# Kernel tuning notes

Measured on AMD Instinct MI355X. Metric: run time of the kernel, lower is better.

Reference implementation:

```python
import jax, jax.numpy as jnp
import numpy as np

B, C, D, H, W = 2, 256, 16, 64, 64


def _conv1x1(x, w, b):
    # 1x1x1 Conv3d == pointwise channel matmul. x: [B,C,D,H,W], w: [Cout,Cin], b: [Cout]
    return jnp.einsum('bcdhw,oc->bodhw', x, w) + b[None, :, None, None, None]


def setup_inputs() -> dict:
    key = jax.random.key(0)
    ks = jax.random.split(key, 12)
    wscale = 1.0 / np.sqrt(C)  # keep pre-softmax logits in a sane range
    inp = {
        'eeg_input': jax.random.normal(ks[0], (B, C, D, H, W), jnp.float32),
        'image_input': jax.random.normal(ks[1], (B, C, D, H, W), jnp.float32),
        'q_w': jax.random.normal(ks[2], (C, C), jnp.float32) * wscale,
        'q_b': jnp.zeros((C,), jnp.float32),
        'k_w': jax.random.normal(ks[3], (C, C), jnp.float32) * wscale,
        'k_b': jnp.zeros((C,), jnp.float32),
        'v_w': jax.random.normal(ks[4], (C, C), jnp.float32) * wscale,
        'v_b': jnp.zeros((C,), jnp.float32),
        'attn_w': jax.random.normal(ks[5], (C, C), jnp.float32) * wscale,
        'attn_b': jnp.zeros((C,), jnp.float32),
        'out_w': jax.random.normal(ks[6], (C, C), jnp.float32) * wscale,
        'out_b': jnp.zeros((C,), jnp.float32),
    }
    return inp


def reference(eeg_input, image_input, q_w, q_b, k_w, k_b, v_w, v_b,
              attn_w, attn_b, out_w, out_b):
    q = _conv1x1(eeg_input, q_w, q_b)      # [B,C,D,H,W]
    k = _conv1x1(image_input, k_w, k_b)    # [B,C,D,H,W]
    v = _conv1x1(image_input, v_w, v_b)    # [B,C,D,H,W]
    # torch.matmul(q, k.transpose(-2,-1)): contract over W -> scores [B,C,D,H,H]
    scores = jax.nn.softmax(jnp.einsum('bcdhw,bcdxw->bcdhx', q, k), axis=-1)
    wv = jnp.einsum('bcdhx,bcdxw->bcdhw', scores, v)  # [B,C,D,H,W]
    a = jax.nn.relu(_conv1x1(wv, attn_w, attn_b))
    return jax.nn.relu(_conv1x1(a, out_w, out_b))
```

## Files before the change

### kernel.cpp

```cpp
#include <hip/hip_runtime.h>

#define CC   256
#define DHWC 65536
#define NBC  2

typedef __attribute__((ext_vector_type(8))) short bf16x8;
typedef __attribute__((ext_vector_type(4))) short bf16x4;
typedef __attribute__((ext_vector_type(4))) float f32x4;

__device__ __forceinline__ short f2bf(float x) {
    unsigned u = __builtin_bit_cast(unsigned, x);
    unsigned r = (u + 0x7fffu + ((u >> 16) & 1u)) >> 16;
    return (short)r;
}
__device__ __forceinline__ float bf2f(short h) {
    unsigned u = ((unsigned)(unsigned short)h) << 16;
    return __builtin_bit_cast(float, u);
}

__device__ __forceinline__ int swz(int r, int c) {
    return (r * 128 + c * 2) ^ ((r & 7) << 4);
}
__device__ __forceinline__ int vswz(int r, int c) {
    return (r * 128 + c * 2) ^ (((r ^ (r >> 3)) & 7) << 4);
}
__device__ __forceinline__ int swz512(int s, int k) {
    return (s * 512 + k * 2) ^ ((s & 7) << 4);
}

__global__ void prep_w_kernel(const float* __restrict__ q_w, const float* __restrict__ k_w,
                              const float* __restrict__ v_w, const float* __restrict__ attn_w,
                              const float* __restrict__ out_w, short* __restrict__ wsp)
{
    const int l  = threadIdx.x;
    const int fo = blockIdx.x;
    const int t  = blockIdx.y;
    const int m  = blockIdx.z;
    const float* w = (m == 0) ? q_w : (m == 1) ? k_w : (m == 2) ? v_w
                   : (m == 3) ? attn_w : out_w;
    short* whi = wsp + (size_t)m * 131072;
    short* wlo = whi + 65536;

    const int o = fo * 16 + (l & 15);
    const int k = t * 32 + (l >> 4) * 8;

    bf16x8 hv, lv;
    #pragma unroll
    for (int r = 0; r < 8; ++r) {
        const float x = w[o * 256 + k + r];
        const short h = f2bf(x);
        hv[r] = h;
        lv[r] = f2bf(x - bf2f(h));
    }
    const int idx = (fo * 8 + t) * 64 + l;
    *(bf16x8*)(whi + idx * 8) = hv;
    *(bf16x8*)(wlo + idx * 8) = lv;
}

__global__ __launch_bounds__(1024, 4) void conv_mfma_kernel(
    const float* __restrict__ x, const short* __restrict__ whi,
    const short* __restrict__ wlo, const float* __restrict__ bias,
    float* __restrict__ out, const int do_relu)
{
    __shared__ char lds[65536];

    const int tid  = threadIdx.x;
    const int lane = tid & 63;
    const int wave = tid >> 6;
    const size_t boff = (size_t)blockIdx.y * ((size_t)CC * DHWC);
    const int sT = blockIdx.x * 128;
    const float* xb = x + boff + sT;
    const bf16x8* whf = (const bf16x8*)whi;
    const bf16x8* wlf = (const bf16x8*)wlo;

    f32x4 acc[8];
    #pragma unroll
    for (int j = 0; j < 8; ++j) acc[j] = (f32x4){0.f, 0.f, 0.f, 0.f};

    const int s_l = tid & 127;
    const int k8  = tid >> 7;

    float xr[8];
    #pragma unroll
    for (int r = 0; r < 8; ++r)
        xr[r] = xb[(size_t)(k8 * 8 + r) * DHWC + s_l];
    {
        bf16x8 hv, lv;
        #pragma unroll
        for (int r = 0; r < 8; ++r) {
            const short h = f2bf(xr[r]);
            hv[r] = h;
            lv[r] = f2bf(xr[r] - bf2f(h));
        }
        const int off = swz(s_l, k8 * 8);
        *(bf16x8*)(lds + off) = hv;
        *(bf16x8*)(lds + 16384 + off) = lv;
    }

    #pragma unroll
    for (int t = 0; t < 4; ++t) {
        if (t < 3) {
            #pragma unroll
            for (int r = 0; r < 8; ++r)
                xr[r] = xb[(size_t)((t + 1) * 64 + k8 * 8 + r) * DHWC + s_l];
        }
        __syncthreads();

        const char* bhib = lds + (t & 1) * 32768;
        const char* blob = bhib + 16384;
        #pragma unroll
        for (int kk = 0; kk < 2; ++kk) {
            const int idx = (wave * 8 + 2 * t + kk) * 64 + lane;
            const bf16x8 a1h = whf[idx];
            const bf16x8 a1l = wlf[idx];
            #pragma unroll
            for (int j = 0; j < 8; ++j) {
                const int s = j * 16 + (lane & 15);
                const int k = kk * 32 + (lane >> 4) * 8;
                const bf16x8 bh = *(const bf16x8*)(bhib + swz(s, k));
                const bf16x8 bl = *(const bf16x8*)(blob + swz(s, k));
                f32x4 c = acc[j];
                c = __builtin_amdgcn_mfma_f32_16x16x32_bf16(a1h, bh, c, 0, 0, 0);
                c = __builtin_amdgcn_mfma_f32_16x16x32_bf16(a1h, bl, c, 0, 0, 0);
                c = __builtin_amdgcn_mfma_f32_16x16x32_bf16(a1l, bh, c, 0, 0, 0);
                acc[j] = c;
            }
        }

        if (t < 3) {
            bf16x8 hv, lv;
            #pragma unroll
            for (int r = 0; r < 8; ++r) {
                const short h = f2bf(xr[r]);
                hv[r] = h;
                lv[r] = f2bf(xr[r] - bf2f(h));
            }
            const int off = ((t + 1) & 1) * 32768 + swz(s_l, k8 * 8);
            *(bf16x8*)(lds + off) = hv;
            *(bf16x8*)(lds + 16384 + off) = lv;
        }
    }

    float* ob = out + boff + sT;
    const int n_l = lane & 15;
    const int m4  = (lane >> 4) * 4;
    #pragma unroll
    for (int r = 0; r < 4; ++r) {
        const int o = wave * 16 + m4 + r;
        const float bv = bias[o];
        #pragma unroll
        for (int j = 0; j < 8; ++j) {
            float val = acc[j][r] + bv;
            if (do_relu) val = fmaxf(val, 0.f);
            ob[(size_t)o * DHWC + j * 16 + n_l] = val;
        }
    }
}

__global__ __launch_bounds__(1024, 4) void kv_conv_kernel(
    const float* __restrict__ img,
    const short* __restrict__ wkhi, const short* __restrict__ wklo,
    const short* __restrict__ wvhi, const short* __restrict__ wvlo,
    const float* __restrict__ kb, const float* __restrict__ vb,
    float* __restrict__ kout, short* __restrict__ vout)
{
    __shared__ char lds[65536];

    const int tid  = threadIdx.x;
    const int lane = tid & 63;
    const int wave = tid >> 6;
    const size_t boff = (size_t)blockIdx.y * ((size_t)CC * DHWC);
    const int sT = blockIdx.x * 128;
    const float* xb = img + boff + sT;
    const bf16x8* wkhf = (const bf16x8*)wkhi;
    const bf16x8* wklf = (const bf16x8*)wklo;
    const bf16x8* wvhf = (const bf16x8*)wvhi;
    const bf16x8* wvlf = (const bf16x8*)wvlo;

    f32x4 acck[8], accv[8];
    #pragma unroll
    for (int j = 0; j < 8; ++j) {
        acck[j] = (f32x4){0.f, 0.f, 0.f, 0.f};
        accv[j] = (f32x4){0.f, 0.f, 0.f, 0.f};
    }

    const int s_l = tid & 127;
    const int k8  = tid >> 7;

    float xr[8];
    #pragma unroll
    for (int r = 0; r < 8; ++r)
        xr[r] = xb[(size_t)(k8 * 8 + r) * DHWC + s_l];
    {
        bf16x8 hv, lv;
        #pragma unroll
        for (int r = 0; r < 8; ++r) {
            const short h = f2bf(xr[r]);
            hv[r] = h;
            lv[r] = f2bf(xr[r] - bf2f(h));
        }
        const int off = swz(s_l, k8 * 8);
        *(bf16x8*)(lds + off) = hv;
        *(bf16x8*)(lds + 16384 + off) = lv;
    }

    #pragma unroll
    for (int t = 0; t < 4; ++t) {
        if (t < 3) {
            #pragma unroll
            for (int r = 0; r < 8; ++r)
                xr[r] = xb[(size_t)((t + 1) * 64 + k8 * 8 + r) * DHWC + s_l];
        }
        __syncthreads();

        const char* bhib = lds + (t & 1) * 32768;
        const char* blob = bhib + 16384;
        #pragma unroll
        for (int kk = 0; kk < 2; ++kk) {
            const int idx = (wave * 8 + 2 * t + kk) * 64 + lane;
            const bf16x8 akh = wkhf[idx];
            const bf16x8 akl = wklf[idx];
            const bf16x8 avh = wvhf[idx];
            const bf16x8 avl = wvlf[idx];
            #pragma unroll
            for (int j = 0; j < 8; ++j) {
                const int s = j * 16 + (lane & 15);
                const int k = kk * 32 + (lane >> 4) * 8;
                const bf16x8 bh = *(const bf16x8*)(bhib + swz(s, k));
                const bf16x8 bl = *(const bf16x8*)(blob + swz(s, k));
                f32x4 c = acck[j];
                c = __builtin_amdgcn_mfma_f32_16x16x32_bf16(akh, bh, c, 0, 0, 0);
                c = __builtin_amdgcn_mfma_f32_16x16x32_bf16(akh, bl, c, 0, 0, 0);
                c = __builtin_amdgcn_mfma_f32_16x16x32_bf16(akl, bh, c, 0, 0, 0);
                acck[j] = c;
                f32x4 d = accv[j];
                d = __builtin_amdgcn_mfma_f32_16x16x32_bf16(avh, bh, d, 0, 0, 0);
                d = __builtin_amdgcn_mfma_f32_16x16x32_bf16(avh, bl, d, 0, 0, 0);
                d = __builtin_amdgcn_mfma_f32_16x16x32_bf16(avl, bh, d, 0, 0, 0);
                accv[j] = d;
            }
        }

        if (t < 3) {
            bf16x8 hv, lv;
            #pragma unroll
            for (int r = 0; r < 8; ++r) {
                const short h = f2bf(xr[r]);
                hv[r] = h;
                lv[r] = f2bf(xr[r] - bf2f(h));
            }
            const int off = ((t + 1) & 1) * 32768 + swz(s_l, k8 * 8);
            *(bf16x8*)(lds + off) = hv;
            *(bf16x8*)(lds + 16384 + off) = lv;
        }
    }

    float* ko = kout + boff + sT;
    short* vo = vout + boff + sT;
    const int n_l = lane & 15;
    const int m4  = (lane >> 4) * 4;
    #pragma unroll
    for (int r = 0; r < 4; ++r) {
        const int o = wave * 16 + m4 + r;
        const float kbv = kb[o];
        const float vbv = vb[o];
        #pragma unroll
        for (int j = 0; j < 8; ++j) {
            ko[(size_t)o * DHWC + j * 16 + n_l] = acck[j][r] + kbv;
            vo[(size_t)o * DHWC + j * 16 + n_l] = f2bf(accv[j][r] + vbv);
        }
    }
}

__global__ __launch_bounds__(256, 4) void attn_mfma_kernel(
    const float* q, const float* __restrict__ kg,
    const short* __restrict__ vsh, float* wv)
{
    __shared__ char lds[40960];
    const int QHI = 0, QLO = 8192, KHI = 16384, KLO = 24576, VT = 32768;

    const int tid  = threadIdx.x;
    const int lane = tid & 63;
    const int wsx  = tid >> 6;
    const size_t base = (size_t)blockIdx.x * 4096;

    {
        const int r  = tid >> 2;
        const int cb = (tid & 3) * 16;
        #pragma unroll
        for (int half = 0; half < 2; ++half) {
            const int c = cb + half * 8;
            const float4 qa = *(const float4*)(q  + base + r * 64 + c);
            const float4 qb = *(const float4*)(q  + base + r * 64 + c + 4);
            const float4 ka = *(const float4*)(kg + base + r * 64 + c);
            const float4 kb = *(const float4*)(kg + base + r * 64 + c + 4);
            bf16x8 qh, ql, kh, kl;
            #pragma unroll
            for (int e = 0; e < 4; ++e) {
                float xq = ((const float*)&qa)[e];
                short h = f2bf(xq); qh[e] = h; ql[e] = f2bf(xq - bf2f(h));
                xq = ((const float*)&qb)[e];
                h = f2bf(xq); qh[e + 4] = h; ql[e + 4] = f2bf(xq - bf2f(h));
                float xk = ((const float*)&ka)[e];
                h = f2bf(xk); kh[e] = h; kl[e] = f2bf(xk - bf2f(h));
                xk = ((const float*)&kb)[e];
                h = f2bf(xk); kh[e + 4] = h; kl[e + 4] = f2bf(xk - bf2f(h));
            }
            const int off = swz(r, c);
            *(bf16x8*)(lds + QHI + off) = qh;
            *(bf16x8*)(lds + QLO + off) = ql;
            *(bf16x8*)(lds + KHI + off) = kh;
            *(bf16x8*)(lds + KLO + off) = kl;
        }
        const short* vpl = vsh + base;
        const int x0 = (tid >> 4) * 4;
        const int w0 = (tid & 15) * 4;
        bf16x4 vr[4];
        #pragma unroll
        for (int i = 0; i < 4; ++i)
            vr[i] = *(const bf16x4*)(vpl + (x0 + i) * 64 + w0);
        #pragma unroll
        for (int j = 0; j < 4; ++j) {
            bf16x4 tv;
            #pragma unroll
            for (int i = 0; i < 4; ++i) tv[i] = vr[i][j];
            *(bf16x4*)(lds + VT + vswz(w0 + j, x0)) = tv;
        }
    }
    __syncthreads();

    f32x4 acc[4];
    #pragma unroll
    for (int j = 0; j < 4; ++j) acc[j] = (f32x4){0.f, 0.f, 0.f, 0.f};

    const int arow = wsx * 16 + (lane & 15);
    #pragma unroll
    for (int kk = 0; kk < 2; ++kk) {
        const int kcol = kk * 32 + (lane >> 4) * 8;
        const bf16x8 aqh = *(const bf16x8*)(lds + QHI + swz(arow, kcol));
        const bf16x8 aql = *(const bf16x8*)(lds + QLO + swz(arow, kcol));
        #pragma unroll
        for (int j = 0; j < 4; ++j) {
            const int brow = j * 16 + (lane & 15);
            const bf16x8 bkh = *(const bf16x8*)(lds + KHI + swz(brow, kcol));
            const bf16x8 bkl = *(const bf16x8*)(lds + KLO + swz(brow, kcol));
            f32x4 c = acc[j];
            c = __builtin_amdgcn_mfma_f32_16x16x32_bf16(aqh, bkh, c, 0, 0, 0);
            c = __builtin_amdgcn_mfma_f32_16x16x32_bf16(aqh, bkl, c, 0, 0, 0);
            c = __builtin_amdgcn_mfma_f32_16x16x32_bf16(aql, bkh, c, 0, 0, 0);
            acc[j] = c;
        }
    }

    float p[4][4], invs[4];
    #pragma unroll
    for (int r = 0; r < 4; ++r) {
        float m = fmaxf(fmaxf(acc[0][r], acc[1][r]), fmaxf(acc[2][r], acc[3][r]));
        m = fmaxf(m, __shfl_xor(m, 1));
        m = fmaxf(m, __shfl_xor(m, 2));
        m = fmaxf(m, __shfl_xor(m, 4));
        m = fmaxf(m, __shfl_xor(m, 8));
        float s = 0.f;
        #pragma unroll
        for (int j = 0; j < 4; ++j) { p[j][r] = __expf(acc[j][r] - m); s += p[j][r]; }
        s += __shfl_xor(s, 1);
        s += __shfl_xor(s, 2);
        s += __shfl_xor(s, 4);
        s += __shfl_xor(s, 8);
        invs[r] = 1.f / s;
    }

    __syncthreads();

    #pragma unroll
    for (int r = 0; r < 4; ++r) {
        const int row = wsx * 16 + (lane >> 4) * 4 + r;
        #pragma unroll
        for (int j = 0; j < 4; ++j) {
            const int col = j * 16 + (lane & 15);
            *(short*)(lds + QHI + swz(row, col)) = f2bf(p[j][r]);
        }
    }
    __syncthreads();

    f32x4 o_[4];
    #pragma unroll
    for (int j = 0; j < 4; ++j) o_[j] = (f32x4){0.f, 0.f, 0.f, 0.f};

    #pragma unroll
    for (int kk = 0; kk < 2; ++kk) {
        const int kcol = kk * 32 + (lane >> 4) * 8;
        const bf16x8 aph = *(const bf16x8*)(lds + QHI + swz(arow, kcol));
        #pragma unroll
        for (int j = 0; j < 4; ++j) {
            const int brow = j * 16 + (lane & 15);
            const bf16x8 bvh = *(const bf16x8*)(lds + VT + vswz(brow, kcol));
            o_[j] = __builtin_amdgcn_mfma_f32_16x16x32_bf16(aph, bvh, o_[j], 0, 0, 0);
        }
    }

    #pragma unroll
    for (int r = 0; r < 4; ++r) {
        const int h = wsx * 16 + (lane >> 4) * 4 + r;
        #pragma unroll
        for (int j = 0; j < 4; ++j)
            wv[base + (size_t)h * 64 + j * 16 + (lane & 15)] = o_[j][r] * invs[r];
    }
}

__global__ __launch_bounds__(1024, 4) void tail_fused_kernel(
    const float* __restrict__ x,
    const short* __restrict__ w1hi, const short* __restrict__ w1lo,
    const float* __restrict__ b1,
    const short* __restrict__ w2hi, const short* __restrict__ w2lo,
    const float* __restrict__ b2,
    float* __restrict__ out)
{
    __shared__ char lds[65536];

    const int tid  = threadIdx.x;
    const int lane = tid & 63;
    const int wave = tid >> 6;
    const size_t boff = (size_t)blockIdx.y * ((size_t)CC * DHWC);
    const int sT = blockIdx.x * 128;
    const float* xb = x + boff + sT;
    const bf16x8* w1hf = (const bf16x8*)w1hi;
    const bf16x8* w1lf = (const bf16x8*)w1lo;

    f32x4 acc[8];
    #pragma unroll
    for (int j = 0; j < 8; ++j) acc[j] = (f32x4){0.f, 0.f, 0.f, 0.f};

    const int s_l = tid & 127;
    const int k8  = tid >> 7;

    float xr[8];
    #pragma unroll
    for (int r = 0; r < 8; ++r)
        xr[r] = xb[(size_t)(k8 * 8 + r) * DHWC + s_l];
    {
        bf16x8 hv, lv;
        #pragma unroll
        for (int r = 0; r < 8; ++r) {
            const short h = f2bf(xr[r]);
            hv[r] = h;
            lv[r] = f2bf(xr[r] - bf2f(h));
        }
        const int off = swz(s_l, k8 * 8);
        *(bf16x8*)(lds + off) = hv;
        *(bf16x8*)(lds + 16384 + off) = lv;
    }

    #pragma unroll
    for (int t = 0; t < 4; ++t) {
        if (t < 3) {
            #pragma unroll
            for (int r = 0; r < 8; ++r)
                xr[r] = xb[(size_t)((t + 1) * 64 + k8 * 8 + r) * DHWC + s_l];
        }
        __syncthreads();

        const char* bhib = lds + (t & 1) * 32768;
        const char* blob = bhib + 16384;
        #pragma unroll
        for (int kk = 0; kk < 2; ++kk) {
            const int idx = (wave * 8 + 2 * t + kk) * 64 + lane;
            const bf16x8 a1h = w1hf[idx];
            const bf16x8 a1l = w1lf[idx];
            #pragma unroll
            for (int j = 0; j < 8; ++j) {
                const int s = j * 16 + (lane & 15);
                const int k = kk * 32 + (lane >> 4) * 8;
                const bf16x8 bh = *(const bf16x8*)(bhib + swz(s, k));
                const bf16x8 bl = *(const bf16x8*)(blob + swz(s, k));
                f32x4 c = acc[j];
                c = __builtin_amdgcn_mfma_f32_16x16x32_bf16(a1h, bh, c, 0, 0, 0);
                c = __builtin_amdgcn_mfma_f32_16x16x32_bf16(a1h, bl, c, 0, 0, 0);
                c = __builtin_amdgcn_mfma_f32_16x16x32_bf16(a1l, bh, c, 0, 0, 0);
                acc[j] = c;
            }
        }

        if (t < 3) {
            bf16x8 hv, lv;
            #pragma unroll
            for (int r = 0; r < 8; ++r) {
                const short h = f2bf(xr[r]);
                hv[r] = h;
                lv[r] = f2bf(xr[r] - bf2f(h));
            }
            const int off = ((t + 1) & 1) * 32768 + swz(s_l, k8 * 8);
            *(bf16x8*)(lds + off) = hv;
            *(bf16x8*)(lds + 16384 + off) = lv;
        }
    }

    __syncthreads();
    {
        const int m4 = (lane >> 4) * 4;
        #pragma unroll
        for (int r = 0; r < 4; ++r) {
            const int o = wave * 16 + m4 + r;
            const float bv = b1[o];
            #pragma unroll
            for (int j = 0; j < 8; ++j) {
                const int s = j * 16 + (lane & 15);
                *(short*)(lds + swz512(s, o)) = f2bf(fmaxf(acc[j][r] + bv, 0.f));
            }
        }
    }
    __syncthreads();

    f32x4 acc2[8];
    #pragma unroll
    for (int j = 0; j < 8; ++j) acc2[j] = (f32x4){0.f, 0.f, 0.f, 0.f};

    const bf16x8* w2hf = (const bf16x8*)w2hi;
    const bf16x8* w2lf = (const bf16x8*)w2lo;
    #pragma unroll
    for (int t2 = 0; t2 < 8; ++t2) {
        const int idx = (wave * 8 + t2) * 64 + lane;
        const bf16x8 a2h = w2hf[idx];
        const bf16x8 a2l = w2lf[idx];
        #pragma unroll
        for (int j = 0; j < 8; ++j) {
            const int s = j * 16 + (lane & 15);
            const int k = t2 * 32 + (lane >> 4) * 8;
            const bf16x8 bh = *(const bf16x8*)(lds + swz512(s, k));
            f32x4 c = acc2[j];
            c = __builtin_amdgcn_mfma_f32_16x16x32_bf16(a2h, bh, c, 0, 0, 0);
            c = __builtin_amdgcn_mfma_f32_16x16x32_bf16(a2l, bh, c, 0, 0, 0);
            acc2[j] = c;
        }
    }

    float* ob = out + boff + sT;
    const int n_l = lane & 15;
    const int m4  = (lane >> 4) * 4;
    #pragma unroll
    for (int r = 0; r < 4; ++r) {
        const int o = wave * 16 + m4 + r;
        const float bv = b2[o];
        #pragma unroll
        for (int j = 0; j < 8; ++j)
            ob[(size_t)o * DHWC + j * 16 + n_l] = fmaxf(acc2[j][r] + bv, 0.f);
    }
}

extern "C" void kernel_launch(void* const* d_in, const int* in_sizes, int n_in,
                              void* d_out, int out_size, void* d_ws, size_t ws_size,
                              hipStream_t stream)
{
    const float* eeg    = (const float*)d_in[0];
    const float* img    = (const float*)d_in[1];
    const float* q_w    = (const float*)d_in[2];
    const float* q_b    = (const float*)d_in[3];
    const float* k_w    = (const float*)d_in[4];
    const float* k_b    = (const float*)d_in[5];
    const float* v_w    = (const float*)d_in[6];
    const float* v_b    = (const float*)d_in[7];
    const float* attn_w = (const float*)d_in[8];
    const float* attn_b = (const float*)d_in[9];
    const float* out_w  = (const float*)d_in[10];
    const float* out_b  = (const float*)d_in[11];

    const size_t N = (size_t)NBC * CC * DHWC;
    float* qbuf = (float*)d_ws;
    float* kbuf = qbuf + N;
    short* wsp  = (short*)(kbuf + N);
    short* vsh  = (short*)d_out;
    float* outp = (float*)d_out;

    hipLaunchKernelGGL(prep_w_kernel, dim3(16, 8, 5), dim3(64), 0, stream,
                       q_w, k_w, v_w, attn_w, out_w, wsp);

    const dim3 cgrid(DHWC / 128, NBC);

    hipLaunchKernelGGL(conv_mfma_kernel, cgrid, dim3(1024), 0, stream,
                       eeg, wsp, wsp + 65536, q_b, qbuf, 0);

    hipLaunchKernelGGL(kv_conv_kernel, cgrid, dim3(1024), 0, stream,
                       img, wsp + 131072, wsp + 131072 + 65536,
                       wsp + 2 * 131072, wsp + 2 * 131072 + 65536,
                       k_b, v_b, kbuf, vsh);

    hipLaunchKernelGGL(attn_mfma_kernel, dim3(NBC * CC * 16), dim3(256), 0, stream,
                       qbuf, kbuf, vsh, qbuf);

    hipLaunchKernelGGL(tail_fused_kernel, cgrid, dim3(1024), 0, stream,
                       qbuf, wsp + 3 * 131072, wsp + 3 * 131072 + 65536, attn_b,
                       wsp + 4 * 131072, wsp + 4 * 131072 + 65536, out_b, outp);
}
```

Before: 410.1 us.

## Store attention output as bf16 and drop low-half MFMA in tail conv

The attention kernel gains a mode that writes its output as bf16, staged through LDS for vectorized coalesced stores, into a separate workspace buffer. The tail kernel then reads bf16 input directly, skipping the hi/lo split and one of three MFMAs per step, and uses half the LDS per stage. The V store in the kv conv kernel is also restaged through LDS for wide coalesced writes. The goal is less memory traffic and compute, at the cost of lower precision on the intermediate activations and a path that depends on workspace size.

```diff
diff --git a/kernel.cpp b/kernel.cpp
--- a/kernel.cpp
+++ b/kernel.cpp
@@ -26,6 +26,9 @@
 }
 __device__ __forceinline__ int swz512(int s, int k) {
     return (s * 512 + k * 2) ^ ((s & 7) << 4);
+}
+__device__ __forceinline__ int swz256(int r, int s) {
+    return (r * 256 + s * 2) ^ ((r & 7) << 4);
 }
 
 __global__ void prep_w_kernel(const float* __restrict__ q_w, const float* __restrict__ k_w,
@@ -60,7 +63,7 @@
 __global__ __launch_bounds__(1024, 4) void conv_mfma_kernel(
     const float* __restrict__ x, const short* __restrict__ whi,
     const short* __restrict__ wlo, const float* __restrict__ bias,
-    float* __restrict__ out, const int do_relu)
+    float* __restrict__ out)
 {
     __shared__ char lds[65536];
 
@@ -149,11 +152,8 @@
         const int o = wave * 16 + m4 + r;
         const float bv = bias[o];
         #pragma unroll
-        for (int j = 0; j < 8; ++j) {
-            float val = acc[j][r] + bv;
-            if (do_relu) val = fmaxf(val, 0.f);
-            ob[(size_t)o * DHWC + j * 16 + n_l] = val;
-        }
+        for (int j = 0; j < 8; ++j)
+            ob[(size_t)o * DHWC + j * 16 + n_l] = acc[j][r] + bv;
     }
 }
 
@@ -256,25 +256,41 @@
     }
 
     float* ko = kout + boff + sT;
-    short* vo = vout + boff + sT;
     const int n_l = lane & 15;
     const int m4  = (lane >> 4) * 4;
     #pragma unroll
     for (int r = 0; r < 4; ++r) {
         const int o = wave * 16 + m4 + r;
         const float kbv = kb[o];
+        #pragma unroll
+        for (int j = 0; j < 8; ++j)
+            ko[(size_t)o * DHWC + j * 16 + n_l] = acck[j][r] + kbv;
+    }
+
+    __syncthreads();
+    #pragma unroll
+    for (int r = 0; r < 4; ++r) {
+        const int o = wave * 16 + m4 + r;
         const float vbv = vb[o];
         #pragma unroll
-        for (int j = 0; j < 8; ++j) {
-            ko[(size_t)o * DHWC + j * 16 + n_l] = acck[j][r] + kbv;
-            vo[(size_t)o * DHWC + j * 16 + n_l] = f2bf(accv[j][r] + vbv);
-        }
-    }
-}
-
+        for (int j = 0; j < 8; ++j)
+            *(short*)(lds + swz256(o, j * 16 + n_l)) = f2bf(accv[j][r] + vbv);
+    }
+    __syncthreads();
+    short* vo = vout + boff + sT;
+    #pragma unroll
+    for (int it = 0; it < 4; ++it) {
+        const int row = it * 64 + wave * 4 + (lane >> 4);
+        const int sc  = (lane & 15) * 8;
+        const bf16x8 v8 = *(const bf16x8*)(lds + swz256(row, sc));
+        *(bf16x8*)(vo + (size_t)row * DHWC + sc) = v8;
+    }
+}
+
+template<int WVM>
 __global__ __launch_bounds__(256, 4) void attn_mfma_kernel(
     const float* q, const float* __restrict__ kg,
-    const short* __restrict__ vsh, float* wv)
+    const short* __restrict__ vsh, float* wvf, short* __restrict__ wvs)
 {
     __shared__ char lds[40960];
     const int QHI = 0, QLO = 8192, KHI = 16384, KLO = 24576, VT = 32768;
@@ -399,17 +415,38 @@
         }
     }
 
-    #pragma unroll
-    for (int r = 0; r < 4; ++r) {
-        const int h = wsx * 16 + (lane >> 4) * 4 + r;
-        #pragma unroll
-        for (int j = 0; j < 4; ++j)
-            wv[base + (size_t)h * 64 + j * 16 + (lane & 15)] = o_[j][r] * invs[r];
-    }
-}
-
+    if (WVM == 0) {
+        #pragma unroll
+        for (int r = 0; r < 4; ++r) {
+            const int h = wsx * 16 + (lane >> 4) * 4 + r;
+            #pragma unroll
+            for (int j = 0; j < 4; ++j)
+                wvf[base + (size_t)h * 64 + j * 16 + (lane & 15)] = o_[j][r] * invs[r];
+        }
+    } else {
+        __syncthreads();
+        #pragma unroll
+        for (int r = 0; r < 4; ++r) {
+            const int h = wsx * 16 + (lane >> 4) * 4 + r;
+            #pragma unroll
+            for (int j = 0; j < 4; ++j)
+                *(short*)(lds + QHI + swz(h, j * 16 + (lane & 15))) = f2bf(o_[j][r] * invs[r]);
+        }
+        __syncthreads();
+        #pragma unroll
+        for (int it = 0; it < 4; ++it) {
+            const int row = it * 16 + (tid >> 4);
+            const int sc  = (tid & 15) * 4;
+            bf16x4 v4;
+            v4 = *(const bf16x4*)(lds + QHI + ((row * 128 + sc * 2) ^ ((row & 7) << 4)));
+            *(bf16x4*)(wvs + base + (size_t)row * 64 + sc) = v4;
+        }
+    }
+}
+
+template<int IM>
 __global__ __launch_bounds__(1024, 4) void tail_fused_kernel(
-    const float* __restrict__ x,
+    const float* __restrict__ xf, const short* __restrict__ xs,
     const short* __restrict__ w1hi, const short* __restrict__ w1lo,
     const float* __restrict__ b1,
     const short* __restrict__ w2hi, const short* __restrict__ w2lo,
@@ -423,7 +460,6 @@
     const int wave = tid >> 6;
     const size_t boff = (size_t)blockIdx.y * ((size_t)CC * DHWC);
     const int sT = blockIdx.x * 128;
-    const float* xb = x + boff + sT;
     const bf16x8* w1hf = (const bf16x8*)w1hi;
     const bf16x8* w1lf = (const bf16x8*)w1lo;
 
@@ -433,12 +469,15 @@
 
     const int s_l = tid & 127;
     const int k8  = tid >> 7;
+    const float* xbf = xf + boff + sT;
+    const short* xbs = xs + boff + sT;
 
     float xr[8];
-    #pragma unroll
-    for (int r = 0; r < 8; ++r)
-        xr[r] = xb[(size_t)(k8 * 8 + r) * DHWC + s_l];
-    {
+    short sr[8];
+    if (IM == 0) {
+        #pragma unroll
+        for (int r = 0; r < 8; ++r)
+            xr[r] = xbf[(size_t)(k8 * 8 + r) * DHWC + s_l];
         bf16x8 hv, lv;
         #pragma unroll
         for (int r = 0; r < 8; ++r) {
@@ -449,18 +488,32 @@
         const int off = swz(s_l, k8 * 8);
         *(bf16x8*)(lds + off) = hv;
         *(bf16x8*)(lds + 16384 + off) = lv;
+    } else {
+        #pragma unroll
+        for (int r = 0; r < 8; ++r)
+            sr[r] = xbs[(size_t)(k8 * 8 + r) * DHWC + s_l];
+        bf16x8 hv;
+        #pragma unroll
+        for (int r = 0; r < 8; ++r) hv[r] = sr[r];
+        *(bf16x8*)(lds + swz(s_l, k8 * 8)) = hv;
     }
 
     #pragma unroll
     for (int t = 0; t < 4; ++t) {
         if (t < 3) {
-            #pragma unroll
-            for (int r = 0; r < 8; ++r)
-                xr[r] = xb[(size_t)((t + 1) * 64 + k8 * 8 + r) * DHWC + s_l];
+            if (IM == 0) {
+                #pragma unroll
+                for (int r = 0; r < 8; ++r)
+                    xr[r] = xbf[(size_t)((t + 1) * 64 + k8 * 8 + r) * DHWC + s_l];
+            } else {
+                #pragma unroll
+                for (int r = 0; r < 8; ++r)
+                    sr[r] = xbs[(size_t)((t + 1) * 64 + k8 * 8 + r) * DHWC + s_l];
+            }
         }
         __syncthreads();
 
-        const char* bhib = lds + (t & 1) * 32768;
+        const char* bhib = lds + (t & 1) * (IM == 0 ? 32768 : 16384);
         const char* blob = bhib + 16384;
         #pragma unroll
         for (int kk = 0; kk < 2; ++kk) {
@@ -472,26 +525,35 @@
                 const int s = j * 16 + (lane & 15);
                 const int k = kk * 32 + (lane >> 4) * 8;
                 const bf16x8 bh = *(const bf16x8*)(bhib + swz(s, k));
-                const bf16x8 bl = *(const bf16x8*)(blob + swz(s, k));
                 f32x4 c = acc[j];
                 c = __builtin_amdgcn_mfma_f32_16x16x32_bf16(a1h, bh, c, 0, 0, 0);
-                c = __builtin_amdgcn_mfma_f32_16x16x32_bf16(a1h, bl, c, 0, 0, 0);
                 c = __builtin_amdgcn_mfma_f32_16x16x32_bf16(a1l, bh, c, 0, 0, 0);
+                if (IM == 0) {
+                    const bf16x8 bl = *(const bf16x8*)(blob + swz(s, k));
+                    c = __builtin_amdgcn_mfma_f32_16x16x32_bf16(a1h, bl, c, 0, 0, 0);
+                }
                 acc[j] = c;
             }
         }
 
         if (t < 3) {
-            bf16x8 hv, lv;
-            #pragma unroll
-            for (int r = 0; r < 8; ++r) {
-                const short h = f2bf(xr[r]);
-                hv[r] = h;
-                lv[r] = f2bf(xr[r] - bf2f(h));
-            }
-            const int off = ((t + 1) & 1) * 32768 + swz(s_l, k8 * 8);
-            *(bf16x8*)(lds + off) = hv;
-            *(bf16x8*)(lds + 16384 + off) = lv;
+            const int off = ((t + 1) & 1) * (IM == 0 ? 32768 : 16384) + swz(s_l, k8 * 8);
+            if (IM == 0) {
+                bf16x8 hv, lv;
+                #pragma unroll
+                for (int r = 0; r < 8; ++r) {
+                    const short h = f2bf(xr[r]);
+                    hv[r] = h;
+                    lv[r] = f2bf(xr[r] - bf2f(h));
+                }
+                *(bf16x8*)(lds + off) = hv;
+                *(bf16x8*)(lds + 16384 + off) = lv;
+            } else {
+                bf16x8 hv;
+                #pragma unroll
+                for (int r = 0; r < 8; ++r) hv[r] = sr[r];
+                *(bf16x8*)(lds + off) = hv;
+            }
         }
     }
 
@@ -567,27 +629,39 @@
     const size_t N = (size_t)NBC * CC * DHWC;
     float* qbuf = (float*)d_ws;
     float* kbuf = qbuf + N;
-    short* wsp  = (short*)(kbuf + N);
+    const size_t need_rich = 4 * N + 4 * N + 2 * N + (size_t)5 * 131072 * 2;
+    const bool rich = (ws_size >= need_rich);
+    short* wvs = rich ? (short*)(kbuf + N) : (short*)nullptr;
+    short* wsp = rich ? (wvs + N) : (short*)(kbuf + N);
     short* vsh  = (short*)d_out;
     float* outp = (float*)d_out;
 
-    hipLaunchKernelGGL(prep_w_kernel, dim3(16, 8, 5), dim3(64), 0, stream,
-                       q_w, k_w, v_w, attn_w, out_w, wsp);
+    prep_w_kernel<<<dim3(16, 8, 5), dim3(64), 0, stream>>>(
+        q_w, k_w, v_w, attn_w, out_w, wsp);
 
     const dim3 cgrid(DHWC / 128, NBC);
 
-    hipLaunchKernelGGL(conv_mfma_kernel, cgrid, dim3(1024), 0, stream,
-                       eeg, wsp, wsp + 65536, q_b, qbuf, 0);
-
-    hipLaunchKernelGGL(kv_conv_kernel, cgrid, dim3(1024), 0, stream,
-                       img, wsp + 131072, wsp + 131072 + 65536,
-                       wsp + 2 * 131072, wsp + 2 * 131072 + 65536,
-                       k_b, v_b, kbuf, vsh);
-
-    hipLaunchKernelGGL(attn_mfma_kernel, dim3(NBC * CC * 16), dim3(256), 0, stream,
-                       qbuf, kbuf, vsh, qbuf);
-
-    hipLaunchKernelGGL(tail_fused_kernel, cgrid, dim3(1024), 0, stream,
-                       qbuf, wsp + 3 * 131072, wsp + 3 * 131072 + 65536, attn_b,
-                       wsp + 4 * 131072, wsp + 4 * 131072 + 65536, out_b, outp);
-}
+    conv_mfma_kernel<<<cgrid, dim3(1024), 0, stream>>>(
+        eeg, wsp, wsp + 65536, q_b, qbuf);
+
+    kv_conv_kernel<<<cgrid, dim3(1024), 0, stream>>>(
+        img, wsp + 131072, wsp + 131072 + 65536,
+        wsp + 2 * 131072, wsp + 2 * 131072 + 65536,
+        k_b, v_b, kbuf, vsh);
+
+    if (rich) {
+        attn_mfma_kernel<1><<<dim3(NBC * CC * 16), dim3(256), 0, stream>>>(
+            qbuf, kbuf, vsh, (float*)nullptr, wvs);
+        tail_fused_kernel<1><<<cgrid, dim3(1024), 0, stream>>>(
+            (const float*)nullptr, wvs,
+            wsp + 3 * 131072, wsp + 3 * 131072 + 65536, attn_b,
+            wsp + 4 * 131072, wsp + 4 * 131072 + 65536, out_b, outp);
+    } else {
+        attn_mfma_kernel<0><<<dim3(NBC * CC * 16), dim3(256), 0, stream>>>(
+            qbuf, kbuf, vsh, qbuf, (short*)nullptr);
+        tail_fused_kernel<0><<<cgrid, dim3(1024), 0, stream>>>(
+            qbuf, (const short*)nullptr,
+            wsp + 3 * 131072, wsp + 3 * 131072 + 65536, attn_b,
+            wsp + 4 * 131072, wsp + 4 * 131072 + 65536, out_b, outp);
+    }
+}
```

After: 392.6 us. 1.04x faster.
